# Kernel tuning notes

Hardware: AMD Instinct MI355X
Metric: run time of the kernel (lower is better)

The kernel has to match this reference:

```python
import jax, jax.numpy as jnp
import numpy as np
from jax import lax

EPS_BN = 1e-5
EPS_ADD = 1e-12


def _bn2d(x, g, b):
    # train-mode BatchNorm2d: stats over (N,H,W), biased variance
    m = x.mean(axis=(0, 2, 3), keepdims=True)
    v = x.var(axis=(0, 2, 3), keepdims=True)
    return (x - m) * lax.rsqrt(v + EPS_BN) * g[None, :, None, None] + b[None, :, None, None]


def _bn1d(x, g, b):
    # train-mode BatchNorm1d on [B,C,L]: stats over (N,L)
    m = x.mean(axis=(0, 2), keepdims=True)
    v = x.var(axis=(0, 2), keepdims=True)
    return (x - m) * lax.rsqrt(v + EPS_BN) * g[None, :, None] + b[None, :, None]


def _addw(w, a, b):
    wr = jax.nn.relu(w)
    wn = wr / (wr.sum() + EPS_ADD)
    return wn[0] * a + wn[1] * b


def setup_inputs() -> dict:
    key = jax.random.key(0)
    B, C, L = 16, 128, 16384
    H = 8
    ks = jax.random.split(key, 16)
    inp = {
        "x": jax.random.normal(ks[0], (B, C, L), dtype=jnp.float32),
        "dw_w": jax.random.normal(ks[1], (3, C, 1, 3, 3), dtype=jnp.float32) * 0.1,
        "bn2_g": jnp.ones((3, C), jnp.float32),
        "bn2_b": jnp.zeros((3, C), jnp.float32),
        "pw_w": jax.random.normal(ks[2], (3, C, C), dtype=jnp.float32) * 0.05,
        "pw_b": jax.random.normal(ks[3], (3, C), dtype=jnp.float32) * 0.02,
        "add_w": jnp.ones((2,), jnp.float32),
        "bn1_g": jnp.ones((C,), jnp.float32),
        "bn1_b": jnp.zeros((C,), jnp.float32),
        "W1": jax.random.normal(ks[4], (C, C // 4), dtype=jnp.float32) * 0.05,
        "b1": jnp.zeros((C // 4,), jnp.float32),
        "W2": jax.random.normal(ks[5], (C // 4, C), dtype=jnp.float32) * 0.05,
        "b2": jnp.zeros((C,), jnp.float32),
        "ffn_add_w": jnp.ones((2,), jnp.float32),
        "ffn_bn_g": jnp.ones((C,), jnp.float32),
        "ffn_bn_b": jnp.zeros((C,), jnp.float32),
        "heads": 8,
    }
    return inp


def reference(x, dw_w, bn2_g, bn2_b, pw_w, pw_b, add_w, bn1_g, bn1_b,
              W1, b1, W2, b2, ffn_add_w, ffn_bn_g, ffn_bn_b, heads):
    B, C, L = x.shape
    S = int(np.sqrt(L))  # static perfect-square side
    maps = x.reshape(B, C, S, S)

    # q (stride 1), k, v (stride 2) branches: depthwise3x3 -> BN2d -> pointwise1x1 -> GELU
    outs = []
    for i, st in enumerate((1, 2, 2)):
        y = lax.conv_general_dilated(
            maps, dw_w[i], window_strides=(st, st), padding=[(1, 1), (1, 1)],
            feature_group_count=C, dimension_numbers=("NCHW", "OIHW", "NCHW"))
        y = _bn2d(y, bn2_g[i], bn2_b[i])
        y = jnp.einsum("oc,bchw->bohw", pw_w[i], y) + pw_b[i][None, :, None, None]
        outs.append(jax.nn.gelu(y, approximate=False))
    q, k, v = outs

    def flat(t):  # [B,C,h,w] -> [B, n, C]
        return t.reshape(t.shape[0], t.shape[1], -1).transpose(0, 2, 1)

    q, k, v = flat(q), flat(k), flat(v)  # q: [B,L,C]; k,v: [B,L/4,C]
    dh = C // heads
    qh = q.reshape(B, -1, heads, dh)
    kh = k.reshape(B, -1, heads, dh)
    vh = v.reshape(B, -1, heads, dh)
    qs = jax.nn.softmax(qh, axis=-1)      # softmax over per-head channel dim
    ks_ = jax.nn.softmax(kh, axis=1)      # softmax over key sequence dim
    kv = jnp.einsum("bnhd,bnhe->bhde", ks_, vh)   # [B,H,dh,dh] tiny
    att = jnp.einsum("blhd,bhde->blhe", qs, kv)   # [B,L,H,dh]
    mhlsa = att.transpose(0, 2, 3, 1).reshape(B, C, L)  # concat heads on channel

    att_out = _bn1d(_addw(add_w, mhlsa, x), bn1_g, bn1_b)  # [B,C,L]

    # FFN on [B,L,C]
    f = jax.nn.gelu(jnp.einsum("blc,cf->blf", att_out.transpose(0, 2, 1), W1) + b1, approximate=False)
    f = jax.nn.gelu(jnp.einsum("blf,fc->blc", f, W2) + b2, approximate=False)
    out = _bn1d(_addw(ffn_add_w, f.transpose(0, 2, 1), att_out), ffn_bn_g, ffn_bn_b)
    return out
```

## Files before the change

### kernel.cpp

```cpp
#include <hip/hip_runtime.h>
#include <hip/hip_bf16.h>
#include <math.h>

#define BB 16
#define CC 128
#define LL 16384
#define SS 128
#define LK 4096
#define NHEAD 8
#define DH 16

typedef __attribute__((ext_vector_type(8))) short short8;
typedef __attribute__((ext_vector_type(4))) float f32x4;

__device__ __forceinline__ float gelu_f(float x) {
    return 0.5f * x * (1.0f + erff(x * 0.70710678118654752f));
}

__device__ __forceinline__ ushort f2bf(float f) {
    __hip_bfloat16 h = __float2bfloat16(f);
    return *(ushort*)&h;
}
__device__ __forceinline__ float bf2f(ushort u) {
    union { unsigned int i; float f; } x; x.i = ((unsigned int)u) << 16; return x.f;
}

__device__ __forceinline__ void block_reduce2(float& s1, float& s2) {
    #pragma unroll
    for (int off = 32; off; off >>= 1) {
        s1 += __shfl_down(s1, off);
        s2 += __shfl_down(s2, off);
    }
    __shared__ float red[2][4];
    int wid = threadIdx.x >> 6, lid = threadIdx.x & 63;
    if (lid == 0) { red[0][wid] = s1; red[1][wid] = s2; }
    __syncthreads();
    if (threadIdx.x == 0) {
        int nw = blockDim.x >> 6;
        float a = 0.f, b = 0.f;
        for (int i = 0; i < nw; i++) { a += red[0][i]; b += red[1][i]; }
        s1 = a; s2 = b;
    }
}

__global__ __launch_bounds__(256) void k_dw(const float* __restrict__ x,
        const float* __restrict__ dw_w,
        ushort* __restrict__ dwq, ushort* __restrict__ dwk, ushort* __restrict__ dwv,
        float* __restrict__ dwstats) {
    int bx = blockIdx.x;
    int cg = bx & 3;
    int oh = (bx >> 2) & 127;
    int b  = bx >> 9;
    __shared__ float xs[3][32][132];
    int tid = threadIdx.x;
    int cl  = tid >> 3;
    int owg = tid & 7;
    int ow0 = owg * 16;
    int c   = cg * 32 + cl;
    bool do_kv = ((oh & 1) == 0);

    float wq[9], wk[9], wv[9];
    const float* wp = dw_w + (size_t)c * 9;
    #pragma unroll
    for (int t = 0; t < 9; t++) wq[t] = wp[t];
    #pragma unroll
    for (int t = 0; t < 9; t++) wk[t] = wp[(size_t)CC * 9 + t];
    #pragma unroll
    for (int t = 0; t < 9; t++) wv[t] = wp[(size_t)2 * CC * 9 + t];

    for (int i = tid; i < 3 * 32 * 32; i += 256) {
        int r = i >> 10;
        int rem = i & 1023;
        int ch = rem >> 5;
        int f4 = rem & 31;
        int ih = oh - 1 + r;
        float4 v = make_float4(0.f, 0.f, 0.f, 0.f);
        if (ih >= 0 && ih < 128)
            v = *(const float4*)(x + ((size_t)b * CC + cg * 32 + ch) * (size_t)LL + ih * SS + f4 * 4);
        *(float4*)&xs[r][ch][f4 * 4] = v;
    }
    if (tid < 96) {
        int r = tid >> 5, ch = tid & 31;
        *(float4*)&xs[r][ch][128] = make_float4(0.f, 0.f, 0.f, 0.f);
    }
    __syncthreads();

    float aq[16], ak[8], av[8];
    #pragma unroll
    for (int j = 0; j < 16; j++) aq[j] = 0.f;
    #pragma unroll
    for (int j = 0; j < 8; j++) { ak[j] = 0.f; av[j] = 0.f; }

    #pragma unroll
    for (int r = 0; r < 3; r++) {
        const float* row = &xs[r][cl][0];
        float g[18];
        g[0] = owg ? row[ow0 - 1] : 0.f;
        float4 v0 = *(const float4*)&row[ow0];
        float4 v1 = *(const float4*)&row[ow0 + 4];
        float4 v2 = *(const float4*)&row[ow0 + 8];
        float4 v3 = *(const float4*)&row[ow0 + 12];
        g[1] = v0.x;  g[2] = v0.y;  g[3] = v0.z;  g[4] = v0.w;
        g[5] = v1.x;  g[6] = v1.y;  g[7] = v1.z;  g[8] = v1.w;
        g[9] = v2.x;  g[10] = v2.y; g[11] = v2.z; g[12] = v2.w;
        g[13] = v3.x; g[14] = v3.y; g[15] = v3.z; g[16] = v3.w;
        g[17] = row[ow0 + 16];
        float w0 = wq[3 * r], w1 = wq[3 * r + 1], w2 = wq[3 * r + 2];
        #pragma unroll
        for (int j = 0; j < 16; j++)
            aq[j] += w0 * g[j] + w1 * g[j + 1] + w2 * g[j + 2];
        if (do_kv) {
            float k0 = wk[3 * r], k1 = wk[3 * r + 1], k2 = wk[3 * r + 2];
            float x0 = wv[3 * r], x1 = wv[3 * r + 1], x2 = wv[3 * r + 2];
            #pragma unroll
            for (int j = 0; j < 8; j++) {
                ak[j] += k0 * g[2 * j] + k1 * g[2 * j + 1] + k2 * g[2 * j + 2];
                av[j] += x0 * g[2 * j] + x1 * g[2 * j + 1] + x2 * g[2 * j + 2];
            }
        }
    }

    {
        size_t qbase = (((size_t)b * 4 + cg) * LL + (size_t)oh * 128) * 32 + cl;
        float s1 = 0.f, s2 = 0.f;
        #pragma unroll
        for (int j = 0; j < 16; j++) {
            ushort u = f2bf(aq[j]);
            float fv = bf2f(u);
            s1 += fv; s2 += fv * fv;
            dwq[qbase + (size_t)(ow0 + j) * 32] = u;
        }
        #pragma unroll
        for (int m = 1; m <= 4; m <<= 1) {
            s1 += __shfl_xor(s1, m);
            s2 += __shfl_xor(s2, m);
        }
        if (owg == 0) {
            atomicAdd(&dwstats[(size_t)c * 2 + 0], s1);
            atomicAdd(&dwstats[(size_t)c * 2 + 1], s2);
        }
    }

    if (do_kv) {
        int ohp = oh >> 1;
        size_t kbase = (((size_t)b * 4 + cg) * LK + (size_t)ohp * 64) * 32 + cl;
        float t1 = 0.f, t2 = 0.f, u1 = 0.f, u2 = 0.f;
        #pragma unroll
        for (int j = 0; j < 8; j++) {
            int owp = owg * 8 + j;
            ushort uk = f2bf(ak[j]);
            float fk = bf2f(uk);
            t1 += fk; t2 += fk * fk;
            dwk[kbase + (size_t)owp * 32] = uk;
            ushort uv = f2bf(av[j]);
            float fv = bf2f(uv);
            u1 += fv; u2 += fv * fv;
            dwv[kbase + (size_t)owp * 32] = uv;
        }
        #pragma unroll
        for (int m = 1; m <= 4; m <<= 1) {
            t1 += __shfl_xor(t1, m); t2 += __shfl_xor(t2, m);
            u1 += __shfl_xor(u1, m); u2 += __shfl_xor(u2, m);
        }
        if (owg == 0) {
            atomicAdd(&dwstats[((size_t)CC + c) * 2 + 0], t1);
            atomicAdd(&dwstats[((size_t)CC + c) * 2 + 1], t2);
            atomicAdd(&dwstats[((size_t)2 * CC + c) * 2 + 0], u1);
            atomicAdd(&dwstats[((size_t)2 * CC + c) * 2 + 1], u2);
        }
    }
}

__global__ void k_finalize_dw(const float* __restrict__ stats, const float* __restrict__ pw_w,
                              const float* __restrict__ pw_b, const float* __restrict__ bn2_g,
                              const float* __restrict__ bn2_b,
                              ushort* __restrict__ effWb, float* __restrict__ effB) {
    int br = blockIdx.x >> 7;
    int o  = blockIdx.x & 127;
    int c  = threadIdx.x;
    float N = (br == 0) ? 262144.f : 65536.f;
    float s1 = stats[(br * CC + c) * 2 + 0];
    float s2 = stats[(br * CC + c) * 2 + 1];
    float m = s1 / N;
    float v = s2 / N - m * m;
    float sc = rsqrtf(v + 1e-5f);
    float A  = bn2_g[br * CC + c] * sc;
    float Bc = bn2_b[br * CC + c] - m * A;
    float w  = pw_w[((size_t)br * CC + o) * CC + c];
    effWb[((size_t)br * CC + o) * CC + c] = f2bf(w * A);
    float pb = w * Bc, dummy = 0.f;
    block_reduce2(pb, dummy);
    if (threadIdx.x == 0) effB[br * CC + o] = pw_b[br * CC + o] + pb;
}

__global__ __launch_bounds__(256) void k_gemm_kv(const ushort* __restrict__ dwk,
        const ushort* __restrict__ dwv, const ushort* __restrict__ effWb,
        const float* __restrict__ effB, float* __restrict__ kbuf, float* __restrict__ vbuf) {
    __shared__ __align__(16) char raw[69632];
    short* As = (short*)raw;
    short* Bs = (short*)(raw + 34816);
    float* Sf = (float*)raw;
    int bx = blockIdx.x;
    int brv = bx >> 9;
    int b = (bx >> 5) & 15;
    int p0 = (bx & 31) * 128;
    const ushort* dw = brv ? dwv : dwk;
    const ushort* Wg = effWb + (size_t)(1 + brv) * CC * CC;
    int tid = threadIdx.x;
    for (int i = tid; i < 2048; i += 256) {
        int row = i >> 4; int f4 = i & 15; int cg = f4 >> 2;
        float4 v = *(const float4*)(dw + (((size_t)b * 4 + cg) * LK + p0 + row) * 32 + (f4 & 3) * 8);
        *(float4*)&As[row * 136 + f4 * 8] = v;
    }
    for (int i = tid; i < 2048; i += 256) {
        int row = i >> 4; int f4 = i & 15;
        float4 v = *(const float4*)(Wg + (size_t)row * 128 + f4 * 8);
        *(float4*)&Bs[row * 136 + f4 * 8] = v;
    }
    __syncthreads();
    int w = tid >> 6, l = tid & 63;
    int m0 = w * 32;
    int la = l & 15, lb = l >> 4;
    f32x4 acc[2][8];
    #pragma unroll
    for (int i = 0; i < 2; i++)
        #pragma unroll
        for (int j = 0; j < 8; j++) acc[i][j] = (f32x4){0.f, 0.f, 0.f, 0.f};
    #pragma unroll
    for (int kt = 0; kt < 4; kt++) {
        int kb = kt * 32 + lb * 8;
        short8 a0 = *(const short8*)&As[(m0 + la) * 136 + kb];
        short8 a1 = *(const short8*)&As[(m0 + 16 + la) * 136 + kb];
        #pragma unroll
        for (int nt = 0; nt < 8; nt++) {
            short8 bf = *(const short8*)&Bs[(nt * 16 + la) * 136 + kb];
            acc[0][nt] = __builtin_amdgcn_mfma_f32_16x16x32_bf16(a0, bf, acc[0][nt], 0, 0, 0);
            acc[1][nt] = __builtin_amdgcn_mfma_f32_16x16x32_bf16(a1, bf, acc[1][nt], 0, 0, 0);
        }
    }
    __syncthreads();
    float bias[8];
    #pragma unroll
    for (int nt = 0; nt < 8; nt++) bias[nt] = effB[(1 + brv) * CC + nt * 16 + la];
    #pragma unroll
    for (int mt = 0; mt < 2; mt++)
        #pragma unroll
        for (int nt = 0; nt < 8; nt++)
            #pragma unroll
            for (int i = 0; i < 4; i++) {
                float vv = acc[mt][nt][i] + bias[nt];
                Sf[(m0 + mt * 16 + lb * 4 + i) * 132 + nt * 16 + la] = gelu_f(vv);
            }
    __syncthreads();
    float* outb = (brv ? vbuf : kbuf) + ((size_t)b * LK + p0) * CC;
    for (int i = tid; i < 4096; i += 256) {
        int row = i >> 5; int c4 = i & 31;
        *(float4*)(outb + (size_t)row * CC + c4 * 4) = *(const float4*)&Sf[row * 132 + c4 * 4];
    }
}

__global__ void k_kv_accum(const float* __restrict__ k_buf, const float* __restrict__ v_buf,
                           float* __restrict__ kv_un, float* __restrict__ ssum) {
    int bx = blockIdx.x;
    int b = bx >> 5;
    int h = (bx >> 2) & 7;
    int sl = bx & 3;
    int n0 = sl * 1024;
    __shared__ float kch[64][16];
    __shared__ float vch[64][16];
    int tid = threadIdx.x;
    int d = tid >> 4, e = tid & 15;
    float acc = 0.f, ss = 0.f;
    for (int ch = 0; ch < 16; ch++) {
        int base = n0 + ch * 64;
        {
            int rr = tid >> 2, c4 = (tid & 3) * 4;
            const float* kp = k_buf + ((size_t)b * LK + base + rr) * CC + h * DH + c4;
            const float* vp = v_buf + ((size_t)b * LK + base + rr) * CC + h * DH + c4;
            float4 kf = *(const float4*)kp;
            float4 vf = *(const float4*)vp;
            kch[rr][c4+0] = __expf(kf.x); kch[rr][c4+1] = __expf(kf.y);
            kch[rr][c4+2] = __expf(kf.z); kch[rr][c4+3] = __expf(kf.w);
            vch[rr][c4+0] = vf.x; vch[rr][c4+1] = vf.y;
            vch[rr][c4+2] = vf.z; vch[rr][c4+3] = vf.w;
        }
        __syncthreads();
        #pragma unroll 8
        for (int rr = 0; rr < 64; rr++) {
            float ek = kch[rr][d];
            acc += ek * vch[rr][e];
            ss += ek;
        }
        __syncthreads();
    }
    atomicAdd(&kv_un[(((size_t)b * NHEAD + h) * DH + d) * DH + e], acc);
    if (e == 0) atomicAdd(&ssum[((size_t)b * NHEAD + h) * DH + d], ss);
}

__global__ void k_kv_div(const float* __restrict__ kv_un, const float* __restrict__ ssum,
                         float* __restrict__ kv) {
    int i = blockIdx.x * 256 + threadIdx.x;
    kv[i] = kv_un[i] / ssum[i >> 4];
}

__global__ __launch_bounds__(256) void k_gemm_q(const ushort* __restrict__ dwq,
        const ushort* __restrict__ effWb, const float* __restrict__ effB,
        const float* __restrict__ kvb, const float* __restrict__ add_w,
        const float* __restrict__ x, float* __restrict__ y1) {
    __shared__ __align__(16) char raw[69632];
    short* As = (short*)raw;
    short* Bs = (short*)(raw + 34816);
    float* Sf = (float*)raw;
    __shared__ float kvs[2048];
    int bx = blockIdx.x;
    int b = bx >> 7;
    int p0 = (bx & 127) * 128;
    int tid = threadIdx.x;
    for (int i = tid; i < 512; i += 256)
        *(float4*)&kvs[i * 4] = *(const float4*)(kvb + (size_t)b * 2048 + i * 4);
    for (int i = tid; i < 2048; i += 256) {
        int row = i >> 4; int f4 = i & 15; int cg = f4 >> 2;
        float4 v = *(const float4*)(dwq + (((size_t)b * 4 + cg) * LL + p0 + row) * 32 + (f4 & 3) * 8);
        *(float4*)&As[row * 136 + f4 * 8] = v;
    }
    for (int i = tid; i < 2048; i += 256) {
        int row = i >> 4; int f4 = i & 15;
        float4 v = *(const float4*)(effWb + (size_t)row * 128 + f4 * 8);
        *(float4*)&Bs[row * 136 + f4 * 8] = v;
    }
    __syncthreads();
    int w = tid >> 6, l = tid & 63;
    int m0 = w * 32;
    int la = l & 15, lb = l >> 4;
    f32x4 acc[2][8];
    #pragma unroll
    for (int i = 0; i < 2; i++)
        #pragma unroll
        for (int j = 0; j < 8; j++) acc[i][j] = (f32x4){0.f, 0.f, 0.f, 0.f};
    #pragma unroll
    for (int kt = 0; kt < 4; kt++) {
        int kb = kt * 32 + lb * 8;
        short8 a0 = *(const short8*)&As[(m0 + la) * 136 + kb];
        short8 a1 = *(const short8*)&As[(m0 + 16 + la) * 136 + kb];
        #pragma unroll
        for (int nt = 0; nt < 8; nt++) {
            short8 bf = *(const short8*)&Bs[(nt * 16 + la) * 136 + kb];
            acc[0][nt] = __builtin_amdgcn_mfma_f32_16x16x32_bf16(a0, bf, acc[0][nt], 0, 0, 0);
            acc[1][nt] = __builtin_amdgcn_mfma_f32_16x16x32_bf16(a1, bf, acc[1][nt], 0, 0, 0);
        }
    }
    __syncthreads();
    float bias[8];
    #pragma unroll
    for (int nt = 0; nt < 8; nt++) bias[nt] = effB[nt * 16 + la];
    #pragma unroll
    for (int mt = 0; mt < 2; mt++)
        #pragma unroll
        for (int nt = 0; nt < 8; nt++)
            #pragma unroll
            for (int i = 0; i < 4; i++) {
                float vv = acc[mt][nt][i] + bias[nt];
                Sf[(m0 + mt * 16 + lb * 4 + i) * 133 + nt * 16 + la] = gelu_f(vv);
            }
    __syncthreads();
    int p = tid & 127;
    int hg = tid >> 7;
    float wa0 = add_w[0], wa1 = add_w[1];
    float r0 = fmaxf(wa0, 0.f), r1 = fmaxf(wa1, 0.f);
    float inv = 1.f / (r0 + r1 + 1e-12f);
    float wn0 = r0 * inv, wn1 = r1 * inv;
    const float* xb = x + (size_t)b * CC * (size_t)LL + p0 + p;
    float* yb = y1 + (size_t)b * CC * (size_t)LL + p0 + p;
    #pragma unroll
    for (int hh = 0; hh < 4; hh++) {
        int h = hg * 4 + hh;
        float sv[16];
        float mx = -1e30f;
        #pragma unroll
        for (int d = 0; d < 16; d++) { sv[d] = Sf[p * 133 + h * 16 + d]; mx = fmaxf(mx, sv[d]); }
        float s = 0.f;
        #pragma unroll
        for (int d = 0; d < 16; d++) { sv[d] = __expf(sv[d] - mx); s += sv[d]; }
        float is = 1.f / s;
        #pragma unroll
        for (int e = 0; e < 16; e++) {
            float att = 0.f;
            #pragma unroll
            for (int d = 0; d < 16; d++) att += sv[d] * kvs[(h * 16 + d) * 16 + e];
            int c = h * 16 + e;
            yb[(size_t)c * LL] = wn0 * att * is + wn1 * xb[(size_t)c * LL];
        }
    }
}

__global__ void k_chan_stats(const float* __restrict__ buf, float* __restrict__ stats) {
    int c = blockIdx.x >> 5;
    int s = blockIdx.x & 31;
    int b = s >> 1;
    int p0 = (s & 1) << 13;
    const float* src = buf + (size_t)b * (CC * (size_t)LL) + (size_t)c * LL + p0;
    float s1 = 0.f, s2 = 0.f;
    for (int i = threadIdx.x * 4; i < 8192; i += 1024) {
        float4 v = *(const float4*)(src + i);
        s1 += v.x + v.y + v.z + v.w;
        s2 += v.x * v.x + v.y * v.y + v.z * v.z + v.w * v.w;
    }
    block_reduce2(s1, s2);
    if (threadIdx.x == 0) {
        atomicAdd(&stats[c * 2 + 0], s1);
        atomicAdd(&stats[c * 2 + 1], s2);
    }
}

__global__ void k_fin1(const float* __restrict__ stats1, const float* __restrict__ bn1_g,
                       const float* __restrict__ bn1_b, const float* __restrict__ W1,
                       const float* __restrict__ b1, const float* __restrict__ W2,
                       float* __restrict__ A1B1, float* __restrict__ effW1,
                       float* __restrict__ effb1, float* __restrict__ W2T) {
    int t = threadIdx.x;
    const float N = 262144.f;
    float m = stats1[t * 2] / N;
    float v = stats1[t * 2 + 1] / N - m * m;
    float sc = rsqrtf(v + 1e-5f);
    float A = bn1_g[t] * sc;
    float Bc = bn1_b[t] - m * A;
    A1B1[t] = A; A1B1[128 + t] = Bc;
    __shared__ float Bs[128];
    Bs[t] = Bc;
    for (int j = 0; j < 32; j++) effW1[t * 32 + j] = W1[t * 32 + j] * A;
    for (int j = 0; j < 32; j++) W2T[t * 32 + j] = W2[j * 128 + t];
    __syncthreads();
    if (t < 32) {
        float s = b1[t];
        for (int c = 0; c < 128; c++) s += W1[c * 32 + t] * Bs[c];
        effb1[t] = s;
    }
}

__global__ __launch_bounds__(256) void k_ffn1(const float* __restrict__ y1,
        const float* __restrict__ effW1, const float* __restrict__ effb1,
        float* __restrict__ f1) {
    __shared__ float wl[4096];
    __shared__ float bl[32];
    int tid = threadIdx.x;
    for (int i = tid; i < 4096; i += 256) wl[i] = effW1[i];
    if (tid < 32) bl[tid] = effb1[tid];
    __syncthreads();
    int gp = blockIdx.x * 256 + tid;
    int b = gp >> 14, p = gp & 16383;
    const float* col = y1 + (size_t)b * (CC * (size_t)LL) + p;
    float acc[32];
    #pragma unroll
    for (int j = 0; j < 32; j++) acc[j] = bl[j];
    for (int c = 0; c < CC; c++) {
        float v = col[(size_t)c * LL];
        const float4* w4 = (const float4*)&wl[c * 32];
        #pragma unroll
        for (int i = 0; i < 8; i++) {
            float4 w = w4[i];
            acc[4*i+0] += w.x * v; acc[4*i+1] += w.y * v;
            acc[4*i+2] += w.z * v; acc[4*i+3] += w.w * v;
        }
    }
    float4* dst = (float4*)(f1 + (size_t)gp * 32);
    #pragma unroll
    for (int i = 0; i < 8; i++) {
        float4 o4;
        o4.x = gelu_f(acc[4*i+0]); o4.y = gelu_f(acc[4*i+1]);
        o4.z = gelu_f(acc[4*i+2]); o4.w = gelu_f(acc[4*i+3]);
        dst[i] = o4;
    }
}

__global__ __launch_bounds__(256) void k_ffn2(const float* __restrict__ f1,
        const float* __restrict__ W2T, const float* __restrict__ b2,
        const float* __restrict__ y1, const float* __restrict__ A1B1,
        const float* __restrict__ ffn_add_w, float* __restrict__ outb) {
    __shared__ float wl[4096];
    __shared__ float b2l[128];
    __shared__ float abl[256];
    int tid = threadIdx.x;
    for (int i = tid; i < 4096; i += 256) wl[i] = W2T[i];
    if (tid < 128) b2l[tid] = b2[tid];
    if (tid >= 128) abl[tid - 128] = A1B1[tid - 128];
    if (tid < 128) abl[128 + tid] = A1B1[128 + tid];
    __syncthreads();
    int gp = blockIdx.x * 256 + tid;
    int b = gp >> 14, p = gp & 16383;
    float f[32];
    {
        const float4* src = (const float4*)(f1 + (size_t)gp * 32);
        #pragma unroll
        for (int i = 0; i < 8; i++) {
            float4 v = src[i];
            f[4*i+0] = v.x; f[4*i+1] = v.y; f[4*i+2] = v.z; f[4*i+3] = v.w;
        }
    }
    float wa0 = ffn_add_w[0], wa1 = ffn_add_w[1];
    float r0 = fmaxf(wa0, 0.f), r1 = fmaxf(wa1, 0.f);
    float inv = 1.f / (r0 + r1 + 1e-12f);
    float wn0 = r0 * inv, wn1 = r1 * inv;
    const float* ycol = y1 + (size_t)b * (CC * (size_t)LL) + p;
    float* ocol = outb + (size_t)b * (CC * (size_t)LL) + p;
    for (int c = 0; c < CC; c++) {
        const float4* w4 = (const float4*)&wl[c * 32];
        float a = b2l[c];
        #pragma unroll
        for (int i = 0; i < 8; i++) {
            float4 w = w4[i];
            a += w.x * f[4*i+0] + w.y * f[4*i+1] + w.z * f[4*i+2] + w.w * f[4*i+3];
        }
        float f2 = gelu_f(a);
        float attv = ycol[(size_t)c * LL] * abl[c] + abl[128 + c];
        ocol[(size_t)c * LL] = wn0 * f2 + wn1 * attv;
    }
}

__global__ void k_fin2(const float* __restrict__ stats2, const float* __restrict__ g,
                       const float* __restrict__ bb, float* __restrict__ A2B2) {
    int t = threadIdx.x;
    const float N = 262144.f;
    float m = stats2[t * 2] / N;
    float v = stats2[t * 2 + 1] / N - m * m;
    float sc = rsqrtf(v + 1e-5f);
    float A = g[t] * sc;
    A2B2[t] = A;
    A2B2[128 + t] = bb[t] - m * A;
}

__global__ void k_norm(float* __restrict__ out, const float* __restrict__ A2B2) {
    size_t i = ((size_t)blockIdx.x * 256 + threadIdx.x) * 4;
    int c = (int)((i >> 14) & 127);
    float A = A2B2[c], Bc = A2B2[128 + c];
    float4 v = *(float4*)(out + i);
    v.x = v.x * A + Bc; v.y = v.y * A + Bc; v.z = v.z * A + Bc; v.w = v.w * A + Bc;
    *(float4*)(out + i) = v;
}

extern "C" void kernel_launch(void* const* d_in, const int* in_sizes, int n_in,
                              void* d_out, int out_size, void* d_ws, size_t ws_size,
                              hipStream_t stream) {
    const float* x        = (const float*)d_in[0];
    const float* dw_w     = (const float*)d_in[1];
    const float* bn2_g    = (const float*)d_in[2];
    const float* bn2_b    = (const float*)d_in[3];
    const float* pw_w     = (const float*)d_in[4];
    const float* pw_b     = (const float*)d_in[5];
    const float* add_w    = (const float*)d_in[6];
    const float* bn1_g    = (const float*)d_in[7];
    const float* bn1_b    = (const float*)d_in[8];
    const float* W1       = (const float*)d_in[9];
    const float* b1       = (const float*)d_in[10];
    const float* W2       = (const float*)d_in[11];
    const float* b2       = (const float*)d_in[12];
    const float* ffn_aw   = (const float*)d_in[13];
    const float* ffn_bn_g = (const float*)d_in[14];
    const float* ffn_bn_b = (const float*)d_in[15];

    float* w = (float*)d_ws;
    size_t off = 0;
    auto alloc = [&](size_t n) { float* p = w + off; off += n; return p; };
    float* dwstats = alloc(768);
    float* stats1  = alloc(256);
    float* stats2  = alloc(256);
    float* kv_un   = alloc(32768);
    float* ssum    = alloc(2048);
    size_t zero_bytes = off * sizeof(float);
    float* effWb_f = alloc(24576);
    float* effB    = alloc(384);
    float* kvb     = alloc(32768);
    float* A1B1    = alloc(256);
    float* effW1   = alloc(4096);
    float* effb1   = alloc(32);
    float* W2T     = alloc(4096);
    float* A2B2    = alloc(256);
    float* y1      = alloc((size_t)BB * CC * LL);
    float* kbuf    = alloc((size_t)BB * LK * CC);
    float* vbuf    = alloc((size_t)BB * LK * CC);
    float* dwq_f   = alloc((size_t)BB * LL * CC / 2);
    float* dwk_f   = alloc((size_t)BB * LK * CC / 2);
    float* dwv_f   = alloc((size_t)BB * LK * CC / 2);
    float* f1      = kbuf;
    (void)ws_size;

    ushort* effWb = (ushort*)effWb_f;
    ushort* dwq = (ushort*)dwq_f;
    ushort* dwk = (ushort*)dwk_f;
    ushort* dwv = (ushort*)dwv_f;
    float* outf = (float*)d_out;

    hipMemsetAsync(d_ws, 0, zero_bytes, stream);

    k_dw<<<8192, 256, 0, stream>>>(x, dw_w, dwq, dwk, dwv, dwstats);
    k_finalize_dw<<<384, 128, 0, stream>>>(dwstats, pw_w, pw_b, bn2_g, bn2_b, effWb, effB);
    k_gemm_kv<<<1024, 256, 0, stream>>>(dwk, dwv, effWb, effB, kbuf, vbuf);
    k_kv_accum<<<512, 256, 0, stream>>>(kbuf, vbuf, kv_un, ssum);
    k_kv_div<<<128, 256, 0, stream>>>(kv_un, ssum, kvb);
    k_gemm_q<<<2048, 256, 0, stream>>>(dwq, effWb, effB, kvb, add_w, x, y1);
    k_chan_stats<<<4096, 256, 0, stream>>>(y1, stats1);
    k_fin1<<<1, 128, 0, stream>>>(stats1, bn1_g, bn1_b, W1, b1, W2, A1B1, effW1, effb1, W2T);
    k_ffn1<<<1024, 256, 0, stream>>>(y1, effW1, effb1, f1);
    k_ffn2<<<1024, 256, 0, stream>>>(f1, W2T, b2, y1, A1B1, ffn_aw, outf);
    k_chan_stats<<<4096, 256, 0, stream>>>(outf, stats2);
    k_fin2<<<1, 128, 0, stream>>>(stats2, ffn_bn_g, ffn_bn_b, A2B2);
    k_norm<<<32768, 256, 0, stream>>>(outf, A2B2);
}
```

Before: 856.1 us.

## Load GEMM operands straight from global and halve the epilogue LDS staging buffer

Both the k/v and q GEMM kernels now read their MFMA A and B fragments directly from global memory instead of first staging them in padded shared-memory tiles. The epilogue writes the GELU results into a 64-row shared buffer in two passes, one per 16-row half of each wave's tile, instead of a 128-row buffer. This cuts LDS use per block from about 68KB to about 34KB, which may allow more resident blocks per CU. The cost is uncoalesced, repeated global reads of the weights and activations through cache, plus extra barriers and a more scattered store pattern in the epilogue.

```diff
diff --git a/kernel.cpp b/kernel.cpp
--- a/kernel.cpp
+++ b/kernel.cpp
@@ -196,10 +196,7 @@
 __global__ __launch_bounds__(256) void k_gemm_kv(const ushort* __restrict__ dwk,
         const ushort* __restrict__ dwv, const ushort* __restrict__ effWb,
         const float* __restrict__ effB, float* __restrict__ kbuf, float* __restrict__ vbuf) {
-    __shared__ __align__(16) char raw[69632];
-    short* As = (short*)raw;
-    short* Bs = (short*)(raw + 34816);
-    float* Sf = (float*)raw;
+    __shared__ __align__(16) float Sf[64 * 132];
     int bx = blockIdx.x;
     int brv = bx >> 9;
     int b = (bx >> 5) & 15;
@@ -207,17 +204,6 @@
     const ushort* dw = brv ? dwv : dwk;
     const ushort* Wg = effWb + (size_t)(1 + brv) * CC * CC;
     int tid = threadIdx.x;
-    for (int i = tid; i < 2048; i += 256) {
-        int row = i >> 4; int f4 = i & 15; int cg = f4 >> 2;
-        float4 v = *(const float4*)(dw + (((size_t)b * 4 + cg) * LK + p0 + row) * 32 + (f4 & 3) * 8);
-        *(float4*)&As[row * 136 + f4 * 8] = v;
-    }
-    for (int i = tid; i < 2048; i += 256) {
-        int row = i >> 4; int f4 = i & 15;
-        float4 v = *(const float4*)(Wg + (size_t)row * 128 + f4 * 8);
-        *(float4*)&Bs[row * 136 + f4 * 8] = v;
-    }
-    __syncthreads();
     int w = tid >> 6, l = tid & 63;
     int m0 = w * 32;
     int la = l & 15, lb = l >> 4;
@@ -228,34 +214,36 @@
         for (int j = 0; j < 8; j++) acc[i][j] = (f32x4){0.f, 0.f, 0.f, 0.f};
     #pragma unroll
     for (int kt = 0; kt < 4; kt++) {
+        short8 a0 = *(const short8*)(dw + (((size_t)b * 4 + kt) * LK + p0 + m0 + la) * 32 + lb * 8);
+        short8 a1 = *(const short8*)(dw + (((size_t)b * 4 + kt) * LK + p0 + m0 + 16 + la) * 32 + lb * 8);
         int kb = kt * 32 + lb * 8;
-        short8 a0 = *(const short8*)&As[(m0 + la) * 136 + kb];
-        short8 a1 = *(const short8*)&As[(m0 + 16 + la) * 136 + kb];
         #pragma unroll
         for (int nt = 0; nt < 8; nt++) {
-            short8 bf = *(const short8*)&Bs[(nt * 16 + la) * 136 + kb];
+            short8 bf = *(const short8*)(Wg + (size_t)(nt * 16 + la) * 128 + kb);
             acc[0][nt] = __builtin_amdgcn_mfma_f32_16x16x32_bf16(a0, bf, acc[0][nt], 0, 0, 0);
             acc[1][nt] = __builtin_amdgcn_mfma_f32_16x16x32_bf16(a1, bf, acc[1][nt], 0, 0, 0);
         }
     }
-    __syncthreads();
     float bias[8];
     #pragma unroll
     for (int nt = 0; nt < 8; nt++) bias[nt] = effB[(1 + brv) * CC + nt * 16 + la];
-    #pragma unroll
-    for (int mt = 0; mt < 2; mt++)
+    float* outb = (brv ? vbuf : kbuf) + ((size_t)b * LK + p0) * CC;
+    #pragma unroll
+    for (int mt = 0; mt < 2; mt++) {
+        __syncthreads();
         #pragma unroll
         for (int nt = 0; nt < 8; nt++)
             #pragma unroll
             for (int i = 0; i < 4; i++) {
                 float vv = acc[mt][nt][i] + bias[nt];
-                Sf[(m0 + mt * 16 + lb * 4 + i) * 132 + nt * 16 + la] = gelu_f(vv);
+                Sf[(w * 16 + lb * 4 + i) * 132 + nt * 16 + la] = gelu_f(vv);
             }
-    __syncthreads();
-    float* outb = (brv ? vbuf : kbuf) + ((size_t)b * LK + p0) * CC;
-    for (int i = tid; i < 4096; i += 256) {
-        int row = i >> 5; int c4 = i & 31;
-        *(float4*)(outb + (size_t)row * CC + c4 * 4) = *(const float4*)&Sf[row * 132 + c4 * 4];
+        __syncthreads();
+        for (int i = tid; i < 2048; i += 256) {
+            int r = i >> 5; int c4 = i & 31;
+            int pact = (r >> 4) * 32 + mt * 16 + (r & 15);
+            *(float4*)(outb + (size_t)pact * CC + c4 * 4) = *(const float4*)&Sf[r * 132 + c4 * 4];
+        }
     }
 }
 
@@ -307,10 +295,7 @@
         const ushort* __restrict__ effWb, const float* __restrict__ effB,
         const float* __restrict__ kvb, const float* __restrict__ add_w,
         const float* __restrict__ x, float* __restrict__ y1) {
-    __shared__ __align__(16) char raw[69632];
-    short* As = (short*)raw;
-    short* Bs = (short*)(raw + 34816);
-    float* Sf = (float*)raw;
+    __shared__ __align__(16) float Sf[64 * 133];
     __shared__ float kvs[2048];
     int bx = blockIdx.x;
     int b = bx >> 7;
@@ -318,17 +303,6 @@
     int tid = threadIdx.x;
     for (int i = tid; i < 512; i += 256)
         *(float4*)&kvs[i * 4] = *(const float4*)(kvb + (size_t)b * 2048 + i * 4);
-    for (int i = tid; i < 2048; i += 256) {
-        int row = i >> 4; int f4 = i & 15; int cg = f4 >> 2;
-        float4 v = *(const float4*)(dwq + (((size_t)b * 4 + cg) * LL + p0 + row) * 32 + (f4 & 3) * 8);
-        *(float4*)&As[row * 136 + f4 * 8] = v;
-    }
-    for (int i = tid; i < 2048; i += 256) {
-        int row = i >> 4; int f4 = i & 15;
-        float4 v = *(const float4*)(effWb + (size_t)row * 128 + f4 * 8);
-        *(float4*)&Bs[row * 136 + f4 * 8] = v;
-    }
-    __syncthreads();
     int w = tid >> 6, l = tid & 63;
     int m0 = w * 32;
     int la = l & 15, lb = l >> 4;
@@ -339,56 +313,58 @@
         for (int j = 0; j < 8; j++) acc[i][j] = (f32x4){0.f, 0.f, 0.f, 0.f};
     #pragma unroll
     for (int kt = 0; kt < 4; kt++) {
+        short8 a0 = *(const short8*)(dwq + (((size_t)b * 4 + kt) * LL + p0 + m0 + la) * 32 + lb * 8);
+        short8 a1 = *(const short8*)(dwq + (((size_t)b * 4 + kt) * LL + p0 + m0 + 16 + la) * 32 + lb * 8);
         int kb = kt * 32 + lb * 8;
-        short8 a0 = *(const short8*)&As[(m0 + la) * 136 + kb];
-        short8 a1 = *(const short8*)&As[(m0 + 16 + la) * 136 + kb];
         #pragma unroll
         for (int nt = 0; nt < 8; nt++) {
-            short8 bf = *(const short8*)&Bs[(nt * 16 + la) * 136 + kb];
+            short8 bf = *(const short8*)(effWb + (size_t)(nt * 16 + la) * 128 + kb);
             acc[0][nt] = __builtin_amdgcn_mfma_f32_16x16x32_bf16(a0, bf, acc[0][nt], 0, 0, 0);
             acc[1][nt] = __builtin_amdgcn_mfma_f32_16x16x32_bf16(a1, bf, acc[1][nt], 0, 0, 0);
         }
     }
-    __syncthreads();
     float bias[8];
     #pragma unroll
     for (int nt = 0; nt < 8; nt++) bias[nt] = effB[nt * 16 + la];
-    #pragma unroll
-    for (int mt = 0; mt < 2; mt++)
+    float wa0 = add_w[0], wa1 = add_w[1];
+    float r0 = fmaxf(wa0, 0.f), r1 = fmaxf(wa1, 0.f);
+    float inv = 1.f / (r0 + r1 + 1e-12f);
+    float wn0 = r0 * inv, wn1 = r1 * inv;
+    #pragma unroll
+    for (int mt = 0; mt < 2; mt++) {
+        __syncthreads();
         #pragma unroll
         for (int nt = 0; nt < 8; nt++)
             #pragma unroll
             for (int i = 0; i < 4; i++) {
                 float vv = acc[mt][nt][i] + bias[nt];
-                Sf[(m0 + mt * 16 + lb * 4 + i) * 133 + nt * 16 + la] = gelu_f(vv);
+                Sf[(w * 16 + lb * 4 + i) * 133 + nt * 16 + la] = gelu_f(vv);
             }
-    __syncthreads();
-    int p = tid & 127;
-    int hg = tid >> 7;
-    float wa0 = add_w[0], wa1 = add_w[1];
-    float r0 = fmaxf(wa0, 0.f), r1 = fmaxf(wa1, 0.f);
-    float inv = 1.f / (r0 + r1 + 1e-12f);
-    float wn0 = r0 * inv, wn1 = r1 * inv;
-    const float* xb = x + (size_t)b * CC * (size_t)LL + p0 + p;
-    float* yb = y1 + (size_t)b * CC * (size_t)LL + p0 + p;
-    #pragma unroll
-    for (int hh = 0; hh < 4; hh++) {
-        int h = hg * 4 + hh;
-        float sv[16];
-        float mx = -1e30f;
-        #pragma unroll
-        for (int d = 0; d < 16; d++) { sv[d] = Sf[p * 133 + h * 16 + d]; mx = fmaxf(mx, sv[d]); }
-        float s = 0.f;
-        #pragma unroll
-        for (int d = 0; d < 16; d++) { sv[d] = __expf(sv[d] - mx); s += sv[d]; }
-        float is = 1.f / s;
-        #pragma unroll
-        for (int e = 0; e < 16; e++) {
-            float att = 0.f;
+        __syncthreads();
+        int r64 = tid & 63;
+        int hg = tid >> 6;
+        int pact = (r64 >> 4) * 32 + mt * 16 + (r64 & 15);
+        const float* xb = x + (size_t)b * CC * (size_t)LL + p0 + pact;
+        float* yb = y1 + (size_t)b * CC * (size_t)LL + p0 + pact;
+        #pragma unroll
+        for (int hh = 0; hh < 2; hh++) {
+            int h = hg * 2 + hh;
+            float sv[16];
+            float mx = -1e30f;
             #pragma unroll
-            for (int d = 0; d < 16; d++) att += sv[d] * kvs[(h * 16 + d) * 16 + e];
-            int c = h * 16 + e;
-            yb[(size_t)c * LL] = wn0 * att * is + wn1 * xb[(size_t)c * LL];
+            for (int d = 0; d < 16; d++) { sv[d] = Sf[r64 * 133 + h * 16 + d]; mx = fmaxf(mx, sv[d]); }
+            float s = 0.f;
+            #pragma unroll
+            for (int d = 0; d < 16; d++) { sv[d] = __expf(sv[d] - mx); s += sv[d]; }
+            float is = 1.f / s;
+            #pragma unroll
+            for (int e = 0; e < 16; e++) {
+                float att = 0.f;
+                #pragma unroll
+                for (int d = 0; d < 16; d++) att += sv[d] * kvs[(h * 16 + d) * 16 + e];
+                int c = h * 16 + e;
+                yb[(size_t)c * LL] = wn0 * att * is + wn1 * xb[(size_t)c * LL];
+            }
         }
     }
 }
```

Result: slower. 997.3 us (+16.5%).
